# Kernel tuning notes

Hardware: AMD Instinct MI355X
Metric: run time of the kernel (lower is better)

Reference implementation:

```python
import jax, jax.numpy as jnp
import numpy as np

ITERATIONS = 4

def setup_inputs() -> dict:
    key = jax.random.key(0)
    x = jax.random.normal(key, (16, 8192, 256), dtype=jnp.float32)
    return {"x": x}

def reference(x):
    # x: [B, S, D]; whiten features (last dim) using stats over axis=1 (sequence)
    B, S, D = x.shape
    m = jnp.mean(x, axis=1, keepdims=True)          # [B, 1, D]
    xn = x - m                                      # centered
    # covariance: [B, D, D]
    sigma = jnp.einsum('bsd,bse->bde', xn, xn) / (S - 1)
    # Newton-Schulz iteration for inverse matrix square root
    tr = jnp.trace(sigma, axis1=1, axis2=2)[:, None, None]   # [B,1,1]
    sigma_n = sigma / tr
    eye = jnp.eye(D, dtype=x.dtype)
    P = jnp.broadcast_to(eye, (B, D, D))
    for _ in range(ITERATIONS):
        P = 1.5 * P - 0.5 * (P @ P @ P @ sigma_n)
    wm = P / jnp.sqrt(tr)                           # whitening matrix [B, D, D]
    decorrelated = jnp.einsum('bsd,bde->bse', xn, wm)
    return decorrelated
```

## Files before the change

### kernel.cpp

```cpp
#include <hip/hip_runtime.h>

#define BB 16
#define SS 8192
#define DD 256

typedef __attribute__((ext_vector_type(8))) short bf16x8;
typedef __attribute__((ext_vector_type(4))) short bf16x4;
typedef __attribute__((ext_vector_type(4))) float f32x4;

union frag_u { bf16x8 v8; bf16x4 v4[2]; };

__device__ __forceinline__ unsigned short f2bf(float f) {
    union { float f; unsigned u; } v; v.f = f;
    unsigned r = v.u + 0x7FFFu + ((v.u >> 16) & 1u);
    return (unsigned short)(r >> 16);
}
__device__ __forceinline__ float bf2f(unsigned short u) {
    union { unsigned u; float f; } cv; cv.u = (unsigned)u << 16; return cv.f;
}
__device__ __forceinline__ unsigned pack2(float a, float b) {
    return (unsigned)f2bf(a) | ((unsigned)f2bf(b) << 16);
}
__device__ __forceinline__ bf16x8 ldfrag(const unsigned short* p) {
    frag_u f;
    f.v4[0] = *(const bf16x4*)(p);
    f.v4[1] = *(const bf16x4*)(p + 4);
    return f.v8;
}
__device__ __forceinline__ void split_bf(float w, unsigned short& hi, unsigned short& lo) {
    hi = f2bf(w);
    lo = f2bf(w - bf2f(hi));
}

#define LTS 40

__global__ __launch_bounds__(512) void moment_kernel(const float* __restrict__ x,
                                                     float* __restrict__ partial,
                                                     float* __restrict__ sumx8) {
    const int kc = blockIdx.x;
    const int nh = blockIdx.y;
    const int b  = blockIdx.z;
    const float* xb = x + ((size_t)b * SS + (size_t)kc * 1024) * DD;

    __shared__ unsigned short Lt0[256 * LTS];
    __shared__ unsigned short Lt1[256 * LTS];
    __shared__ float csh[8 * 256];

    const int tid  = threadIdx.x;
    const int wave = tid >> 6;
    const int lane = tid & 63;
    const int lc   = lane & 15;
    const int lq   = lane >> 4;

    const int mrow0 = (wave & 3) * 64;
    const int ncol0 = nh * 128 + (wave >> 2) * 64;

    const int sg = tid >> 6;
    const int dg = tid & 63;
    const float* xt = xb + (size_t)(sg * 4) * DD + dg;

    f32x4 acc[4][4];
#pragma unroll
    for (int mi = 0; mi < 4; ++mi)
#pragma unroll
        for (int ni = 0; ni < 4; ++ni) acc[mi][ni] = (f32x4){0.f, 0.f, 0.f, 0.f};
    float cs[4] = {0.f, 0.f, 0.f, 0.f};

    float va[16], vb[16];

    auto LOAD = [&](float* v, int t) {
#pragma unroll
        for (int i = 0; i < 4; ++i)
#pragma unroll
            for (int j = 0; j < 4; ++j)
                v[i * 4 + j] = xt[(size_t)(t * 32 + i) * DD + 64 * j];
    };
    auto STAGE = [&](const float* v, unsigned short* Lw) {
        if (nh == 0) {
#pragma unroll
            for (int j = 0; j < 4; ++j)
                cs[j] += v[j] + v[4 + j] + v[8 + j] + v[12 + j];
        }
#pragma unroll
        for (int j = 0; j < 4; ++j) {
            uint2 w;
            w.x = pack2(v[j], v[4 + j]);
            w.y = pack2(v[8 + j], v[12 + j]);
            *(uint2*)&Lw[(dg + 64 * j) * LTS + sg * 4] = w;
        }
    };
    auto COMPUTE = [&](const unsigned short* Lr) {
        bf16x8 af[4], bfr[4];
#pragma unroll
        for (int mi = 0; mi < 4; ++mi)
            af[mi] = *(const bf16x8*)&Lr[(mrow0 + mi * 16 + lc) * LTS + lq * 8];
#pragma unroll
        for (int ni = 0; ni < 4; ++ni)
            bfr[ni] = *(const bf16x8*)&Lr[(ncol0 + ni * 16 + lc) * LTS + lq * 8];
#pragma unroll
        for (int mi = 0; mi < 4; ++mi)
#pragma unroll
            for (int ni = 0; ni < 4; ++ni)
                acc[mi][ni] = __builtin_amdgcn_mfma_f32_16x16x32_bf16(
                    af[mi], bfr[ni], acc[mi][ni], 0, 0, 0);
    };

    LOAD(va, 0);
    STAGE(va, Lt0);
    LOAD(vb, 1);
    __syncthreads();

    for (int tt = 0; tt < 16; ++tt) {
        const int t0 = 2 * tt;
        STAGE(vb, Lt1);
        if (t0 < 30) LOAD(va, t0 + 2);
        COMPUTE(Lt0);
        __syncthreads();
        if (t0 + 1 < 31) STAGE(va, Lt0);
        if (t0 + 1 < 30) LOAD(vb, t0 + 3);
        COMPUTE(Lt1);
        __syncthreads();
    }

    float* pp = partial + (size_t)(kc * 16 + b) * DD * DD;
#pragma unroll
    for (int mi = 0; mi < 4; ++mi)
#pragma unroll
        for (int ni = 0; ni < 4; ++ni) {
            const int row = mrow0 + mi * 16 + lq * 4;
            const int col = ncol0 + ni * 16 + lc;
#pragma unroll
            for (int r = 0; r < 4; ++r)
                pp[(size_t)(row + r) * DD + col] = acc[mi][ni][r];
        }

    if (nh == 0) {
        __syncthreads();
#pragma unroll
        for (int j = 0; j < 4; ++j) csh[sg * 256 + dg + 64 * j] = cs[j];
        __syncthreads();
        if (tid < 256) {
            float t0 = 0.f;
#pragma unroll
            for (int g = 0; g < 8; ++g) t0 += csh[g * 256 + tid];
            sumx8[(size_t)(kc * 16 + b) * DD + tid] = t0;
        }
    }
}

__global__ __launch_bounds__(256) void stats_kernel(const float* __restrict__ partial,
                                                    const float* __restrict__ sumx8,
                                                    float* __restrict__ m,
                                                    float* __restrict__ trbuf) {
    const int b = blockIdx.x;
    const int d = threadIdx.x;
    float sx = 0.f;
#pragma unroll
    for (int kc = 0; kc < 8; ++kc)
        sx += sumx8[(size_t)(kc * 16 + b) * DD + d];
    const float mean = sx * (1.0f / (float)SS);
    m[b * DD + d] = mean;
    float ds = 0.f;
#pragma unroll
    for (int kc = 0; kc < 8; ++kc)
        ds += partial[((size_t)(kc * 16 + b) * DD + d) * DD + d];
    const float diag = (ds - (float)SS * mean * mean) * (1.0f / (float)(SS - 1));
    __shared__ float red[256];
    red[d] = diag;
    __syncthreads();
    for (int off = 128; off > 0; off >>= 1) {
        if (d < off) red[d] += red[d + off];
        __syncthreads();
    }
    if (d == 0) {
        const float tr = red[0];
        trbuf[b]      = tr;
        trbuf[16 + b] = rsqrtf(tr);
        trbuf[32 + b] = 1.0f / tr;
    }
}

__global__ __launch_bounds__(256) void sigman_kernel(const float* __restrict__ partial,
                                                     const float* __restrict__ m,
                                                     const float* __restrict__ trbuf,
                                                     float* __restrict__ Xa) {
    const int b = blockIdx.y;
    const int d = blockIdx.x;
    const int e = threadIdx.x;
    const float itr = trbuf[32 + b];
    const float md = m[b * DD + d];
    const float me = m[b * DD + e];
    float s = 0.f;
#pragma unroll
    for (int kc = 0; kc < 8; ++kc)
        s += partial[((size_t)(kc * 16 + b) * DD + d) * DD + e];
    Xa[(size_t)b * DD * DD + (size_t)d * DD + e] =
        (s - (float)SS * md * me) * (1.0f / (float)(SS - 1)) * itr;
}

#define BTS 72
__global__ __launch_bounds__(256) void bmm_mfma(
    const float* __restrict__ A0, const float* __restrict__ B0, float* __restrict__ C0,
    int ta0, int tb0,
    const float* __restrict__ A1, const float* __restrict__ B1, float* __restrict__ C1,
    int ta1, int tb1) {
    const int by  = blockIdx.y;
    const int set = by >> 4;
    const int bb  = by & 15;
    const float* Ag = (set ? A1 : A0) + (size_t)bb * DD * DD;
    const float* Bg = (set ? B1 : B0) + (size_t)bb * DD * DD;
    float*       Cg = (set ? C1 : C0) + (size_t)bb * DD * DD;
    const int TA = set ? ta1 : ta0;
    const int TB = set ? tb1 : tb0;

    const int m0 = (blockIdx.x >> 2) * 64;
    const int n0 = (blockIdx.x & 3) * 64;

    __shared__ unsigned short Ahi[2][64 * BTS];
    __shared__ unsigned short Alo[2][64 * BTS];
    __shared__ unsigned short Bhi[2][64 * BTS];
    __shared__ unsigned short Blo[2][64 * BTS];

    const int tid  = threadIdx.x;
    const int wave = tid >> 6;
    const int lane = tid & 63;
    const int lc = lane & 15, lq = lane >> 4;
    const int mrow0 = (wave & 1) * 32;
    const int ncol0 = (wave >> 1) * 32;

    const int r  = tid >> 2;
    const int kl = (tid & 3) * 4;
    const float* Arow = Ag + (size_t)(m0 + r) * DD + kl;
    const float* Brow = Bg + (size_t)(n0 + r) * DD + kl;

    f32x4 acc[2][2];
#pragma unroll
    for (int mi = 0; mi < 2; ++mi)
#pragma unroll
        for (int ni = 0; ni < 2; ++ni) acc[mi][ni] = (f32x4){0.f, 0.f, 0.f, 0.f};

    float4 va0[4], vb0[4], va1[4], vb1[4];

    auto LOADC = [&](float4* va, float4* vb, int c) {
#pragma unroll
        for (int i = 0; i < 4; ++i) va[i] = *(const float4*)(Arow + c * 64 + i * 16);
#pragma unroll
        for (int i = 0; i < 4; ++i) vb[i] = *(const float4*)(Brow + c * 64 + i * 16);
    };
    auto STAGE_SIDE = [&](const float4* v, unsigned short* Shi, unsigned short* Slo,
                          int c, int gmn, int tflag) {
#pragma unroll
        for (int i = 0; i < 4; ++i) {
            float xv[4] = {v[i].x, v[i].y, v[i].z, v[i].w};
            unsigned short h[4], l[4];
#pragma unroll
            for (int j = 0; j < 4; ++j) {
                float wv = xv[j];
                if (tflag) {
                    const int gk = c * 64 + kl + i * 16 + j;
                    wv = ((gk == gmn) ? 1.5f : 0.0f) - 0.5f * wv;
                }
                split_bf(wv, h[j], l[j]);
            }
            unsigned short* ph = &Shi[r * BTS + kl + i * 16];
            *(unsigned*)&ph[0] = (unsigned)h[0] | ((unsigned)h[1] << 16);
            *(unsigned*)&ph[2] = (unsigned)h[2] | ((unsigned)h[3] << 16);
            unsigned short* pl = &Slo[r * BTS + kl + i * 16];
            *(unsigned*)&pl[0] = (unsigned)l[0] | ((unsigned)l[1] << 16);
            *(unsigned*)&pl[2] = (unsigned)l[2] | ((unsigned)l[3] << 16);
        }
    };
    auto STAGE = [&](const float4* va, const float4* vb, int c, int buf) {
        STAGE_SIDE(va, Ahi[buf], Alo[buf], c, m0 + r, TA);
        STAGE_SIDE(vb, Bhi[buf], Blo[buf], c, n0 + r, TB);
    };
    auto COMPUTE = [&](int buf) {
#pragma unroll
        for (int ks = 0; ks < 2; ++ks) {
            bf16x8 ah[2], al[2], bh[2], bl[2];
#pragma unroll
            for (int mi = 0; mi < 2; ++mi) {
                const int off = (mrow0 + mi * 16 + lc) * BTS + ks * 32 + lq * 8;
                ah[mi] = *(const bf16x8*)&Ahi[buf][off];
                al[mi] = *(const bf16x8*)&Alo[buf][off];
            }
#pragma unroll
            for (int ni = 0; ni < 2; ++ni) {
                const int off = (ncol0 + ni * 16 + lc) * BTS + ks * 32 + lq * 8;
                bh[ni] = *(const bf16x8*)&Bhi[buf][off];
                bl[ni] = *(const bf16x8*)&Blo[buf][off];
            }
#pragma unroll
            for (int mi = 0; mi < 2; ++mi)
#pragma unroll
                for (int ni = 0; ni < 2; ++ni) {
                    acc[mi][ni] = __builtin_amdgcn_mfma_f32_16x16x32_bf16(
                        al[mi], bh[ni], acc[mi][ni], 0, 0, 0);
                    acc[mi][ni] = __builtin_amdgcn_mfma_f32_16x16x32_bf16(
                        ah[mi], bl[ni], acc[mi][ni], 0, 0, 0);
                    acc[mi][ni] = __builtin_amdgcn_mfma_f32_16x16x32_bf16(
                        ah[mi], bh[ni], acc[mi][ni], 0, 0, 0);
                }
        }
    };

    LOADC(va0, vb0, 0);
    STAGE(va0, vb0, 0, 0);
    LOADC(va1, vb1, 1);
    __syncthreads();
#pragma unroll
    for (int cc = 0; cc < 2; ++cc) {
        const int c0 = 2 * cc;
        STAGE(va1, vb1, c0 + 1, 1);
        if (c0 + 2 < 4) LOADC(va0, vb0, c0 + 2);
        COMPUTE(0);
        __syncthreads();
        if (c0 + 2 < 4) STAGE(va0, vb0, c0 + 2, 0);
        if (c0 + 3 < 4) LOADC(va1, vb1, c0 + 3);
        COMPUTE(1);
        __syncthreads();
    }

#pragma unroll
    for (int mi = 0; mi < 2; ++mi)
#pragma unroll
        for (int ni = 0; ni < 2; ++ni) {
            const int row = m0 + mrow0 + mi * 16 + lq * 4;
            const int col = n0 + ncol0 + ni * 16 + lc;
#pragma unroll
            for (int rr = 0; rr < 4; ++rr)
                Cg[(size_t)(row + rr) * DD + col] = acc[mi][ni][rr];
        }
}

#define BSS 260
__global__ __launch_bounds__(512) void apply_kernel(const float* __restrict__ x,
                                                    const float* __restrict__ P,
                                                    const float* __restrict__ m,
                                                    const float* __restrict__ trbuf,
                                                    float* __restrict__ out) {
    const int st = blockIdx.x;
    const int nh = blockIdx.y;
    const int b  = blockIdx.z;
    const int s0 = st * 256;
    const int n0 = nh * 128;
    const float rs = trbuf[16 + b];
    const float* xb = x + (size_t)b * SS * DD;
    const float* Pb = P + (size_t)b * DD * DD;
    const float* mb = m + b * DD;
    float* ob = out + (size_t)b * SS * DD;

    __shared__ unsigned short Bs[128 * BSS];
    __shared__ unsigned short As0[256 * LTS];
    __shared__ unsigned short As1[256 * LTS];
    __shared__ float corr[128];

    const int tid  = threadIdx.x;
    const int wave = tid >> 6;
    const int lane = tid & 63;
    const int lc = lane & 15, lq = lane >> 4;
    const int mrow0 = (wave & 3) * 64;
    const int ncol0 = (wave >> 2) * 64;

    {
        const int r = tid >> 2, h = tid & 3;
        const float* prow = Pb + (size_t)(n0 + r) * DD + h * 64;
        unsigned short* brow = &Bs[r * BSS + h * 64];
#pragma unroll
        for (int i = 0; i < 16; ++i) {
            float4 pv = *(const float4*)(prow + i * 4);
            *(unsigned*)&brow[i * 4]     = pack2(pv.x * rs, pv.y * rs);
            *(unsigned*)&brow[i * 4 + 2] = pack2(pv.z * rs, pv.w * rs);
        }
    }
    __syncthreads();

    if (tid < 128) {
        float s = 0.f;
        for (int k = 0; k < 256; ++k)
            s += mb[k] * bf2f(Bs[tid * BSS + k]);
        corr[tid] = s;
    }

    f32x4 acc[4][4];
#pragma unroll
    for (int mi = 0; mi < 4; ++mi)
#pragma unroll
        for (int ni = 0; ni < 4; ++ni) acc[mi][ni] = (f32x4){0.f, 0.f, 0.f, 0.f};

    const int r8 = tid >> 3;
    const int d4 = (tid & 7) * 4;
    const float* xt = xb + (size_t)(s0 + r8) * DD + d4;

    float4 va[4], vb[4];

    auto LOAD = [&](float4* v, int t) {
#pragma unroll
        for (int i = 0; i < 4; ++i)
            v[i] = *(const float4*)(xt + (size_t)t * 32 + (size_t)i * 64 * DD);
    };
    auto STAGE = [&](const float4* v, unsigned short* Aw) {
#pragma unroll
        for (int i = 0; i < 4; ++i) {
            uint2 w;
            w.x = pack2(v[i].x, v[i].y);
            w.y = pack2(v[i].z, v[i].w);
            *(uint2*)&Aw[(r8 + i * 64) * LTS + d4] = w;
        }
    };
    auto COMPUTE = [&](const unsigned short* Ar, int t) {
        const int k0 = t * 32;
        bf16x8 af[4], bfr[4];
#pragma unroll
        for (int mi = 0; mi < 4; ++mi)
            af[mi] = *(const bf16x8*)&Ar[(mrow0 + mi * 16 + lc) * LTS + lq * 8];
#pragma unroll
        for (int ni = 0; ni < 4; ++ni)
            bfr[ni] = ldfrag(&Bs[(ncol0 + ni * 16 + lc) * BSS + k0 + lq * 8]);
#pragma unroll
        for (int mi = 0; mi < 4; ++mi)
#pragma unroll
            for (int ni = 0; ni < 4; ++ni)
                acc[mi][ni] = __builtin_amdgcn_mfma_f32_16x16x32_bf16(
                    af[mi], bfr[ni], acc[mi][ni], 0, 0, 0);
    };

    LOAD(va, 0);
    STAGE(va, As0);
    LOAD(vb, 1);
    __syncthreads();

#pragma unroll
    for (int tt = 0; tt < 4; ++tt) {
        const int t0 = 2 * tt;
        STAGE(vb, As1);
        if (t0 < 6) LOAD(va, t0 + 2);
        COMPUTE(As0, t0);
        __syncthreads();
        if (t0 + 2 < 8) STAGE(va, As0);
        if (t0 + 3 < 8) LOAD(vb, t0 + 3);
        COMPUTE(As1, t0 + 1);
        __syncthreads();
    }

#pragma unroll
    for (int mi = 0; mi < 4; ++mi)
#pragma unroll
        for (int ni = 0; ni < 4; ++ni) {
            const int row = s0 + mrow0 + mi * 16 + lq * 4;
            const int col = n0 + ncol0 + ni * 16 + lc;
            const float cv = corr[ncol0 + ni * 16 + lc];
#pragma unroll
            for (int r = 0; r < 4; ++r)
                ob[(size_t)(row + r) * DD + col] = acc[mi][ni][r] - cv;
        }
}

extern "C" void kernel_launch(void* const* d_in, const int* in_sizes, int n_in,
                              void* d_out, int out_size, void* d_ws, size_t ws_size,
                              hipStream_t stream) {
    const float* x = (const float*)d_in[0];
    float* out = (float*)d_out;
    float* ws = (float*)d_ws;

    const size_t MAT = (size_t)BB * DD * DD;
    float* partial = ws;
    float* sumx8 = partial + 8 * MAT;
    float* m     = sumx8 + 8 * BB * DD;
    float* trbuf = m + BB * DD;
    float* Xa    = trbuf + 64;
    float* Xb    = Xa + MAT;
    float* T     = Xb + MAT;
    float* Pa    = T + MAT;
    float* Pb    = Pa + MAT;

    moment_kernel<<<dim3(8, 2, 16), 512, 0, stream>>>(x, partial, sumx8);
    stats_kernel<<<16, 256, 0, stream>>>(partial, sumx8, m, trbuf);
    sigman_kernel<<<dim3(256, 16), 256, 0, stream>>>(partial, m, trbuf, Xa);

    bmm_mfma<<<dim3(16, 16), 256, 0, stream>>>(Xa, Xa, T, 1, 1,
                                               Xa, Xa, T, 1, 1);
    bmm_mfma<<<dim3(16, 16), 256, 0, stream>>>(Xa, T, Xb, 0, 0,
                                               Xa, T, Xb, 0, 0);
    bmm_mfma<<<dim3(16, 32), 256, 0, stream>>>(Xa, Xb, Pa, 1, 1,
                                               Xb, Xb, T, 1, 1);
    bmm_mfma<<<dim3(16, 16), 256, 0, stream>>>(Xb, T, Xa, 0, 0,
                                               Xb, T, Xa, 0, 0);
    bmm_mfma<<<dim3(16, 32), 256, 0, stream>>>(Pa, Xa, Pb, 0, 1,
                                               Xa, Xa, T, 1, 1);
    bmm_mfma<<<dim3(16, 16), 256, 0, stream>>>(Xa, T, Xb, 0, 0,
                                               Xa, T, Xb, 0, 0);
    bmm_mfma<<<dim3(16, 16), 256, 0, stream>>>(Pb, Xb, Pa, 0, 1,
                                               Pb, Xb, Pa, 0, 1);

    apply_kernel<<<dim3(32, 2, 16), 512, 0, stream>>>(x, Pa, m, trbuf, out);
}
```

Measured before the change: 372.8 us.

## Fuse Newton-Schulz matmul chain into one cooperative kernel and retile apply

Replaces the seven separate batched-matmul launches with a single cooperative kernel. It runs nine 64x64-tile passes separated by grid-wide syncs, using 512 threads per block and 8-element staging per thread. The goal is to remove per-launch overhead and tail gaps between the small matmuls. The trade-off is that independent matmul pairs now run one after another and each pass pays a grid-barrier cost. The apply kernel is also retiled to 128-row tiles with 256 threads and a single-buffered A tile, and its B stride is padded so fragments load as aligned 16-byte reads.

```diff
diff --git a/kernel.cpp b/kernel.cpp
--- a/kernel.cpp
+++ b/kernel.cpp
@@ -1,4 +1,7 @@
 #include <hip/hip_runtime.h>
+#include <hip/hip_cooperative_groups.h>
+
+namespace cg = cooperative_groups;
 
 #define BB 16
 #define SS 8192
@@ -7,8 +10,6 @@
 typedef __attribute__((ext_vector_type(8))) short bf16x8;
 typedef __attribute__((ext_vector_type(4))) short bf16x4;
 typedef __attribute__((ext_vector_type(4))) float f32x4;
-
-union frag_u { bf16x8 v8; bf16x4 v4[2]; };
 
 __device__ __forceinline__ unsigned short f2bf(float f) {
     union { float f; unsigned u; } v; v.f = f;
@@ -20,12 +21,6 @@
 }
 __device__ __forceinline__ unsigned pack2(float a, float b) {
     return (unsigned)f2bf(a) | ((unsigned)f2bf(b) << 16);
-}
-__device__ __forceinline__ bf16x8 ldfrag(const unsigned short* p) {
-    frag_u f;
-    f.v4[0] = *(const bf16x4*)(p);
-    f.v4[1] = *(const bf16x4*)(p + 4);
-    return f.v8;
 }
 __device__ __forceinline__ void split_bf(float w, unsigned short& hi, unsigned short& lo) {
     hi = f2bf(w);
@@ -199,142 +194,141 @@
 }
 
 #define BTS 72
-__global__ __launch_bounds__(256) void bmm_mfma(
-    const float* __restrict__ A0, const float* __restrict__ B0, float* __restrict__ C0,
-    int ta0, int tb0,
-    const float* __restrict__ A1, const float* __restrict__ B1, float* __restrict__ C1,
-    int ta1, int tb1) {
-    const int by  = blockIdx.y;
-    const int set = by >> 4;
-    const int bb  = by & 15;
-    const float* Ag = (set ? A1 : A0) + (size_t)bb * DD * DD;
-    const float* Bg = (set ? B1 : B0) + (size_t)bb * DD * DD;
-    float*       Cg = (set ? C1 : C0) + (size_t)bb * DD * DD;
-    const int TA = set ? ta1 : ta0;
-    const int TB = set ? tb1 : tb0;
-
-    const int m0 = (blockIdx.x >> 2) * 64;
-    const int n0 = (blockIdx.x & 3) * 64;
-
-    __shared__ unsigned short Ahi[2][64 * BTS];
-    __shared__ unsigned short Alo[2][64 * BTS];
-    __shared__ unsigned short Bhi[2][64 * BTS];
-    __shared__ unsigned short Blo[2][64 * BTS];
-
+__device__ __forceinline__ void bmm_pass(const float* Ag, const float* Bg, float* Cg,
+                                         int TA, int TB, int tile,
+                                         unsigned short* sm) {
     const int tid  = threadIdx.x;
     const int wave = tid >> 6;
     const int lane = tid & 63;
     const int lc = lane & 15, lq = lane >> 4;
+    const int m0 = (tile >> 2) * 64, n0 = (tile & 3) * 64;
     const int mrow0 = (wave & 1) * 32;
-    const int ncol0 = (wave >> 1) * 32;
-
-    const int r  = tid >> 2;
-    const int kl = (tid & 3) * 4;
-    const float* Arow = Ag + (size_t)(m0 + r) * DD + kl;
-    const float* Brow = Bg + (size_t)(n0 + r) * DD + kl;
-
-    f32x4 acc[2][2];
-#pragma unroll
-    for (int mi = 0; mi < 2; ++mi)
-#pragma unroll
-        for (int ni = 0; ni < 2; ++ni) acc[mi][ni] = (f32x4){0.f, 0.f, 0.f, 0.f};
-
-    float4 va0[4], vb0[4], va1[4], vb1[4];
-
-    auto LOADC = [&](float4* va, float4* vb, int c) {
-#pragma unroll
-        for (int i = 0; i < 4; ++i) va[i] = *(const float4*)(Arow + c * 64 + i * 16);
-#pragma unroll
-        for (int i = 0; i < 4; ++i) vb[i] = *(const float4*)(Brow + c * 64 + i * 16);
-    };
-    auto STAGE_SIDE = [&](const float4* v, unsigned short* Shi, unsigned short* Slo,
-                          int c, int gmn, int tflag) {
-#pragma unroll
-        for (int i = 0; i < 4; ++i) {
-            float xv[4] = {v[i].x, v[i].y, v[i].z, v[i].w};
-            unsigned short h[4], l[4];
-#pragma unroll
-            for (int j = 0; j < 4; ++j) {
-                float wv = xv[j];
-                if (tflag) {
-                    const int gk = c * 64 + kl + i * 16 + j;
-                    wv = ((gk == gmn) ? 1.5f : 0.0f) - 0.5f * wv;
-                }
-                split_bf(wv, h[j], l[j]);
+    const int ncol0 = (wave >> 1) * 16;
+
+    const int r  = tid >> 3;
+    const int k8 = (tid & 7) * 8;
+    const float* Arow = Ag + (size_t)(m0 + r) * DD + k8;
+    const float* Brow = Bg + (size_t)(n0 + r) * DD + k8;
+
+    unsigned short* SL[2][4];
+#pragma unroll
+    for (int bf = 0; bf < 2; ++bf)
+#pragma unroll
+        for (int w = 0; w < 4; ++w) SL[bf][w] = sm + (size_t)(bf * 4 + w) * 64 * BTS;
+
+    f32x4 acc[2];
+    acc[0] = (f32x4){0.f, 0.f, 0.f, 0.f};
+    acc[1] = (f32x4){0.f, 0.f, 0.f, 0.f};
+
+    float4 a0[2], b0[2], a1[2], b1[2];
+
+    auto LOADC = [&](float4* a, float4* b, int c) {
+        a[0] = *(const float4*)(Arow + c * 64);
+        a[1] = *(const float4*)(Arow + c * 64 + 4);
+        b[0] = *(const float4*)(Brow + c * 64);
+        b[1] = *(const float4*)(Brow + c * 64 + 4);
+    };
+    auto STAGE1 = [&](const float4* v, unsigned short* Shi, unsigned short* Slo,
+                      int c, int gmn, int tf) {
+        const float* vf = (const float*)v;
+        unsigned short h[8], l[8];
+#pragma unroll
+        for (int j = 0; j < 8; ++j) {
+            float wv = vf[j];
+            if (tf) {
+                const int gk = c * 64 + k8 + j;
+                wv = ((gk == gmn) ? 1.5f : 0.0f) - 0.5f * wv;
             }
-            unsigned short* ph = &Shi[r * BTS + kl + i * 16];
-            *(unsigned*)&ph[0] = (unsigned)h[0] | ((unsigned)h[1] << 16);
-            *(unsigned*)&ph[2] = (unsigned)h[2] | ((unsigned)h[3] << 16);
-            unsigned short* pl = &Slo[r * BTS + kl + i * 16];
-            *(unsigned*)&pl[0] = (unsigned)l[0] | ((unsigned)l[1] << 16);
-            *(unsigned*)&pl[2] = (unsigned)l[2] | ((unsigned)l[3] << 16);
-        }
-    };
-    auto STAGE = [&](const float4* va, const float4* vb, int c, int buf) {
-        STAGE_SIDE(va, Ahi[buf], Alo[buf], c, m0 + r, TA);
-        STAGE_SIDE(vb, Bhi[buf], Blo[buf], c, n0 + r, TB);
-    };
-    auto COMPUTE = [&](int buf) {
+            split_bf(wv, h[j], l[j]);
+        }
+        uint4 uh, ul;
+        uh.x = (unsigned)h[0] | ((unsigned)h[1] << 16);
+        uh.y = (unsigned)h[2] | ((unsigned)h[3] << 16);
+        uh.z = (unsigned)h[4] | ((unsigned)h[5] << 16);
+        uh.w = (unsigned)h[6] | ((unsigned)h[7] << 16);
+        ul.x = (unsigned)l[0] | ((unsigned)l[1] << 16);
+        ul.y = (unsigned)l[2] | ((unsigned)l[3] << 16);
+        ul.z = (unsigned)l[4] | ((unsigned)l[5] << 16);
+        ul.w = (unsigned)l[6] | ((unsigned)l[7] << 16);
+        *(uint4*)&Shi[r * BTS + k8] = uh;
+        *(uint4*)&Slo[r * BTS + k8] = ul;
+    };
+    auto STAGE = [&](const float4* a, const float4* b, int c, int bf) {
+        STAGE1(a, SL[bf][0], SL[bf][1], c, m0 + r, TA);
+        STAGE1(b, SL[bf][2], SL[bf][3], c, n0 + r, TB);
+    };
+    auto COMPUTE = [&](int bf) {
 #pragma unroll
         for (int ks = 0; ks < 2; ++ks) {
-            bf16x8 ah[2], al[2], bh[2], bl[2];
-#pragma unroll
-            for (int mi = 0; mi < 2; ++mi) {
-                const int off = (mrow0 + mi * 16 + lc) * BTS + ks * 32 + lq * 8;
-                ah[mi] = *(const bf16x8*)&Ahi[buf][off];
-                al[mi] = *(const bf16x8*)&Alo[buf][off];
-            }
-#pragma unroll
-            for (int ni = 0; ni < 2; ++ni) {
-                const int off = (ncol0 + ni * 16 + lc) * BTS + ks * 32 + lq * 8;
-                bh[ni] = *(const bf16x8*)&Bhi[buf][off];
-                bl[ni] = *(const bf16x8*)&Blo[buf][off];
-            }
-#pragma unroll
-            for (int mi = 0; mi < 2; ++mi)
-#pragma unroll
-                for (int ni = 0; ni < 2; ++ni) {
-                    acc[mi][ni] = __builtin_amdgcn_mfma_f32_16x16x32_bf16(
-                        al[mi], bh[ni], acc[mi][ni], 0, 0, 0);
-                    acc[mi][ni] = __builtin_amdgcn_mfma_f32_16x16x32_bf16(
-                        ah[mi], bl[ni], acc[mi][ni], 0, 0, 0);
-                    acc[mi][ni] = __builtin_amdgcn_mfma_f32_16x16x32_bf16(
-                        ah[mi], bh[ni], acc[mi][ni], 0, 0, 0);
-                }
-        }
-    };
-
-    LOADC(va0, vb0, 0);
-    STAGE(va0, vb0, 0, 0);
-    LOADC(va1, vb1, 1);
+            const int ko = ks * 32 + lq * 8;
+            bf16x8 ah0 = *(const bf16x8*)&SL[bf][0][(mrow0 + lc) * BTS + ko];
+            bf16x8 ah1 = *(const bf16x8*)&SL[bf][0][(mrow0 + 16 + lc) * BTS + ko];
+            bf16x8 al0 = *(const bf16x8*)&SL[bf][1][(mrow0 + lc) * BTS + ko];
+            bf16x8 al1 = *(const bf16x8*)&SL[bf][1][(mrow0 + 16 + lc) * BTS + ko];
+            bf16x8 bh  = *(const bf16x8*)&SL[bf][2][(ncol0 + lc) * BTS + ko];
+            bf16x8 bl  = *(const bf16x8*)&SL[bf][3][(ncol0 + lc) * BTS + ko];
+            acc[0] = __builtin_amdgcn_mfma_f32_16x16x32_bf16(al0, bh, acc[0], 0, 0, 0);
+            acc[0] = __builtin_amdgcn_mfma_f32_16x16x32_bf16(ah0, bl, acc[0], 0, 0, 0);
+            acc[0] = __builtin_amdgcn_mfma_f32_16x16x32_bf16(ah0, bh, acc[0], 0, 0, 0);
+            acc[1] = __builtin_amdgcn_mfma_f32_16x16x32_bf16(al1, bh, acc[1], 0, 0, 0);
+            acc[1] = __builtin_amdgcn_mfma_f32_16x16x32_bf16(ah1, bl, acc[1], 0, 0, 0);
+            acc[1] = __builtin_amdgcn_mfma_f32_16x16x32_bf16(ah1, bh, acc[1], 0, 0, 0);
+        }
+    };
+
+    LOADC(a0, b0, 0);
+    STAGE(a0, b0, 0, 0);
+    LOADC(a1, b1, 1);
     __syncthreads();
 #pragma unroll
     for (int cc = 0; cc < 2; ++cc) {
         const int c0 = 2 * cc;
-        STAGE(va1, vb1, c0 + 1, 1);
-        if (c0 + 2 < 4) LOADC(va0, vb0, c0 + 2);
+        STAGE(a1, b1, c0 + 1, 1);
+        if (c0 + 2 < 4) LOADC(a0, b0, c0 + 2);
         COMPUTE(0);
         __syncthreads();
-        if (c0 + 2 < 4) STAGE(va0, vb0, c0 + 2, 0);
-        if (c0 + 3 < 4) LOADC(va1, vb1, c0 + 3);
+        if (c0 + 2 < 4) STAGE(a0, b0, c0 + 2, 0);
+        if (c0 + 3 < 4) LOADC(a1, b1, c0 + 3);
         COMPUTE(1);
         __syncthreads();
     }
 
 #pragma unroll
-    for (int mi = 0; mi < 2; ++mi)
-#pragma unroll
-        for (int ni = 0; ni < 2; ++ni) {
-            const int row = m0 + mrow0 + mi * 16 + lq * 4;
-            const int col = n0 + ncol0 + ni * 16 + lc;
-#pragma unroll
-            for (int rr = 0; rr < 4; ++rr)
-                Cg[(size_t)(row + rr) * DD + col] = acc[mi][ni][rr];
-        }
-}
-
-#define BSS 260
-__global__ __launch_bounds__(512) void apply_kernel(const float* __restrict__ x,
+    for (int mi = 0; mi < 2; ++mi) {
+        const int row = m0 + mrow0 + mi * 16 + lq * 4;
+        const int col = n0 + ncol0 + lc;
+#pragma unroll
+        for (int rr = 0; rr < 4; ++rr)
+            Cg[(size_t)(row + rr) * DD + col] = acc[mi][rr];
+    }
+}
+
+__global__ __launch_bounds__(512) void ns_chain(float* Xa, float* Xb, float* T,
+                                                float* Pa, float* Pb) {
+    cg::grid_group grid = cg::this_grid();
+    __shared__ __align__(16) unsigned short sm[8 * 64 * BTS];
+
+    const int bx   = blockIdx.x;
+    const int tile = bx & 15;
+    const size_t off = (size_t)(bx >> 4) * DD * DD;
+
+    const float* Al[9] = {Xa, Xa, Xa, Xb, Xb, Pa, Xa, Xa, Pb};
+    const float* Bl[9] = {Xa, T,  Xb, Xb, T,  Xa, Xa, T,  Xb};
+    float*       Cl[9] = {T,  Xb, Pa, T,  Xa, Pb, T,  Xb, Pa};
+    const int   TAl[9] = {1, 0, 1, 1, 0, 0, 1, 0, 0};
+    const int   TBl[9] = {1, 0, 1, 1, 0, 1, 1, 0, 1};
+
+    for (int p = 0; p < 9; ++p) {
+        if (p) {
+            __threadfence();
+            grid.sync();
+        }
+        bmm_pass(Al[p] + off, Bl[p] + off, Cl[p] + off, TAl[p], TBl[p], tile, sm);
+    }
+}
+
+#define BSS 264
+__global__ __launch_bounds__(256) void apply_kernel(const float* __restrict__ x,
                                                     const float* __restrict__ P,
                                                     const float* __restrict__ m,
                                                     const float* __restrict__ trbuf,
@@ -342,7 +336,7 @@
     const int st = blockIdx.x;
     const int nh = blockIdx.y;
     const int b  = blockIdx.z;
-    const int s0 = st * 256;
+    const int s0 = st * 128;
     const int n0 = nh * 128;
     const float rs = trbuf[16 + b];
     const float* xb = x + (size_t)b * SS * DD;
@@ -351,23 +345,22 @@
     float* ob = out + (size_t)b * SS * DD;
 
     __shared__ unsigned short Bs[128 * BSS];
-    __shared__ unsigned short As0[256 * LTS];
-    __shared__ unsigned short As1[256 * LTS];
+    __shared__ unsigned short As[128 * LTS];
     __shared__ float corr[128];
 
     const int tid  = threadIdx.x;
     const int wave = tid >> 6;
     const int lane = tid & 63;
     const int lc = lane & 15, lq = lane >> 4;
-    const int mrow0 = (wave & 3) * 64;
-    const int ncol0 = (wave >> 2) * 64;
+    const int mrow0 = (wave & 1) * 64;
+    const int ncol0 = (wave >> 1) * 64;
 
     {
-        const int r = tid >> 2, h = tid & 3;
-        const float* prow = Pb + (size_t)(n0 + r) * DD + h * 64;
-        unsigned short* brow = &Bs[r * BSS + h * 64];
-#pragma unroll
-        for (int i = 0; i < 16; ++i) {
+        const int r = tid >> 1, h = tid & 1;
+        const float* prow = Pb + (size_t)(n0 + r) * DD + h * 128;
+        unsigned short* brow = &Bs[r * BSS + h * 128];
+#pragma unroll
+        for (int i = 0; i < 32; ++i) {
             float4 pv = *(const float4*)(prow + i * 4);
             *(unsigned*)&brow[i * 4]     = pack2(pv.x * rs, pv.y * rs);
             *(unsigned*)&brow[i * 4 + 2] = pack2(pv.z * rs, pv.w * rs);
@@ -397,26 +390,26 @@
     auto LOAD = [&](float4* v, int t) {
 #pragma unroll
         for (int i = 0; i < 4; ++i)
-            v[i] = *(const float4*)(xt + (size_t)t * 32 + (size_t)i * 64 * DD);
-    };
-    auto STAGE = [&](const float4* v, unsigned short* Aw) {
+            v[i] = *(const float4*)(xt + (size_t)t * 32 + (size_t)i * 32 * DD);
+    };
+    auto STAGE = [&](const float4* v) {
 #pragma unroll
         for (int i = 0; i < 4; ++i) {
             uint2 w;
             w.x = pack2(v[i].x, v[i].y);
             w.y = pack2(v[i].z, v[i].w);
-            *(uint2*)&Aw[(r8 + i * 64) * LTS + d4] = w;
-        }
-    };
-    auto COMPUTE = [&](const unsigned short* Ar, int t) {
+            *(uint2*)&As[(r8 + i * 32) * LTS + d4] = w;
+        }
+    };
+    auto COMPUTE = [&](int t) {
         const int k0 = t * 32;
         bf16x8 af[4], bfr[4];
 #pragma unroll
         for (int mi = 0; mi < 4; ++mi)
-            af[mi] = *(const bf16x8*)&Ar[(mrow0 + mi * 16 + lc) * LTS + lq * 8];
+            af[mi] = *(const bf16x8*)&As[(mrow0 + mi * 16 + lc) * LTS + lq * 8];
 #pragma unroll
         for (int ni = 0; ni < 4; ++ni)
-            bfr[ni] = ldfrag(&Bs[(ncol0 + ni * 16 + lc) * BSS + k0 + lq * 8]);
+            bfr[ni] = *(const bf16x8*)&Bs[(ncol0 + ni * 16 + lc) * BSS + k0 + lq * 8];
 #pragma unroll
         for (int mi = 0; mi < 4; ++mi)
 #pragma unroll
@@ -426,21 +419,19 @@
     };
 
     LOAD(va, 0);
-    STAGE(va, As0);
-    LOAD(vb, 1);
-    __syncthreads();
-
 #pragma unroll
     for (int tt = 0; tt < 4; ++tt) {
         const int t0 = 2 * tt;
-        STAGE(vb, As1);
-        if (t0 < 6) LOAD(va, t0 + 2);
-        COMPUTE(As0, t0);
-        __syncthreads();
-        if (t0 + 2 < 8) STAGE(va, As0);
-        if (t0 + 3 < 8) LOAD(vb, t0 + 3);
-        COMPUTE(As1, t0 + 1);
-        __syncthreads();
+        __syncthreads();
+        STAGE(va);
+        if (t0 + 1 < 8) LOAD(vb, t0 + 1);
+        __syncthreads();
+        COMPUTE(t0);
+        __syncthreads();
+        STAGE(vb);
+        if (t0 + 2 < 8) LOAD(va, t0 + 2);
+        __syncthreads();
+        COMPUTE(t0 + 1);
     }
 
 #pragma unroll
@@ -478,20 +469,10 @@
     stats_kernel<<<16, 256, 0, stream>>>(partial, sumx8, m, trbuf);
     sigman_kernel<<<dim3(256, 16), 256, 0, stream>>>(partial, m, trbuf, Xa);
 
-    bmm_mfma<<<dim3(16, 16), 256, 0, stream>>>(Xa, Xa, T, 1, 1,
-                                               Xa, Xa, T, 1, 1);
-    bmm_mfma<<<dim3(16, 16), 256, 0, stream>>>(Xa, T, Xb, 0, 0,
-                                               Xa, T, Xb, 0, 0);
-    bmm_mfma<<<dim3(16, 32), 256, 0, stream>>>(Xa, Xb, Pa, 1, 1,
-                                               Xb, Xb, T, 1, 1);
-    bmm_mfma<<<dim3(16, 16), 256, 0, stream>>>(Xb, T, Xa, 0, 0,
-                                               Xb, T, Xa, 0, 0);
-    bmm_mfma<<<dim3(16, 32), 256, 0, stream>>>(Pa, Xa, Pb, 0, 1,
-                                               Xa, Xa, T, 1, 1);
-    bmm_mfma<<<dim3(16, 16), 256, 0, stream>>>(Xa, T, Xb, 0, 0,
-                                               Xa, T, Xb, 0, 0);
-    bmm_mfma<<<dim3(16, 16), 256, 0, stream>>>(Pb, Xb, Pa, 0, 1,
-                                               Pb, Xb, Pa, 0, 1);
-
-    apply_kernel<<<dim3(32, 2, 16), 512, 0, stream>>>(x, Pa, m, trbuf, out);
-}
+    {
+        void* args[] = {&Xa, &Xb, &T, &Pa, &Pb};
+        hipLaunchCooperativeKernel(ns_chain, dim3(256), dim3(512), args, 0, stream);
+    }
+
+    apply_kernel<<<dim3(64, 2, 16), 256, 0, stream>>>(x, Pa, m, trbuf, out);
+}
```

Result: slower. 987.3 us (+164.8%).

## Shrink apply kernel tiles to 128 rows with single LDS buffer

Applied to the files above, without the earlier changes.

The apply kernel now processes 128 sequence rows per block with 256 threads (4 waves) instead of 256 rows with 512 threads, doubling the grid and dropping the double-buffered A tile for a single buffer with extra barriers. The B tile stride is padded to 264 so B fragments can be read with a single 16-byte LDS load instead of two 8-byte loads. The intent is lower LDS use per block, more resident blocks and better tail balance. The cost is that each block re-converts the P slice for half as many rows and loses compute/staging overlap within the block. The bmm kernel also issues its second global load before the first staging.

```diff
diff --git a/kernel.cpp b/kernel.cpp
--- a/kernel.cpp
+++ b/kernel.cpp
@@ -7,8 +7,6 @@
 typedef __attribute__((ext_vector_type(8))) short bf16x8;
 typedef __attribute__((ext_vector_type(4))) short bf16x4;
 typedef __attribute__((ext_vector_type(4))) float f32x4;
-
-union frag_u { bf16x8 v8; bf16x4 v4[2]; };
 
 __device__ __forceinline__ unsigned short f2bf(float f) {
     union { float f; unsigned u; } v; v.f = f;
@@ -20,12 +18,6 @@
 }
 __device__ __forceinline__ unsigned pack2(float a, float b) {
     return (unsigned)f2bf(a) | ((unsigned)f2bf(b) << 16);
-}
-__device__ __forceinline__ bf16x8 ldfrag(const unsigned short* p) {
-    frag_u f;
-    f.v4[0] = *(const bf16x4*)(p);
-    f.v4[1] = *(const bf16x4*)(p + 4);
-    return f.v8;
 }
 __device__ __forceinline__ void split_bf(float w, unsigned short& hi, unsigned short& lo) {
     hi = f2bf(w);
@@ -305,8 +297,8 @@
     };
 
     LOADC(va0, vb0, 0);
+    LOADC(va1, vb1, 1);
     STAGE(va0, vb0, 0, 0);
-    LOADC(va1, vb1, 1);
     __syncthreads();
 #pragma unroll
     for (int cc = 0; cc < 2; ++cc) {
@@ -333,8 +325,8 @@
         }
 }
 
-#define BSS 260
-__global__ __launch_bounds__(512) void apply_kernel(const float* __restrict__ x,
+#define BSS 264
+__global__ __launch_bounds__(256) void apply_kernel(const float* __restrict__ x,
                                                     const float* __restrict__ P,
                                                     const float* __restrict__ m,
                                                     const float* __restrict__ trbuf,
@@ -342,7 +334,7 @@
     const int st = blockIdx.x;
     const int nh = blockIdx.y;
     const int b  = blockIdx.z;
-    const int s0 = st * 256;
+    const int s0 = st * 128;
     const int n0 = nh * 128;
     const float rs = trbuf[16 + b];
     const float* xb = x + (size_t)b * SS * DD;
@@ -351,23 +343,22 @@
     float* ob = out + (size_t)b * SS * DD;
 
     __shared__ unsigned short Bs[128 * BSS];
-    __shared__ unsigned short As0[256 * LTS];
-    __shared__ unsigned short As1[256 * LTS];
+    __shared__ unsigned short As[128 * LTS];
     __shared__ float corr[128];
 
     const int tid  = threadIdx.x;
     const int wave = tid >> 6;
     const int lane = tid & 63;
     const int lc = lane & 15, lq = lane >> 4;
-    const int mrow0 = (wave & 3) * 64;
-    const int ncol0 = (wave >> 2) * 64;
+    const int mrow0 = (wave & 1) * 64;
+    const int ncol0 = (wave >> 1) * 64;
 
     {
-        const int r = tid >> 2, h = tid & 3;
-        const float* prow = Pb + (size_t)(n0 + r) * DD + h * 64;
-        unsigned short* brow = &Bs[r * BSS + h * 64];
-#pragma unroll
-        for (int i = 0; i < 16; ++i) {
+        const int r = tid >> 1, h = tid & 1;
+        const float* prow = Pb + (size_t)(n0 + r) * DD + h * 128;
+        unsigned short* brow = &Bs[r * BSS + h * 128];
+#pragma unroll
+        for (int i = 0; i < 32; ++i) {
             float4 pv = *(const float4*)(prow + i * 4);
             *(unsigned*)&brow[i * 4]     = pack2(pv.x * rs, pv.y * rs);
             *(unsigned*)&brow[i * 4 + 2] = pack2(pv.z * rs, pv.w * rs);
@@ -397,26 +388,26 @@
     auto LOAD = [&](float4* v, int t) {
 #pragma unroll
         for (int i = 0; i < 4; ++i)
-            v[i] = *(const float4*)(xt + (size_t)t * 32 + (size_t)i * 64 * DD);
-    };
-    auto STAGE = [&](const float4* v, unsigned short* Aw) {
+            v[i] = *(const float4*)(xt + (size_t)t * 32 + (size_t)i * 32 * DD);
+    };
+    auto STAGE = [&](const float4* v) {
 #pragma unroll
         for (int i = 0; i < 4; ++i) {
             uint2 w;
             w.x = pack2(v[i].x, v[i].y);
             w.y = pack2(v[i].z, v[i].w);
-            *(uint2*)&Aw[(r8 + i * 64) * LTS + d4] = w;
-        }
-    };
-    auto COMPUTE = [&](const unsigned short* Ar, int t) {
+            *(uint2*)&As[(r8 + i * 32) * LTS + d4] = w;
+        }
+    };
+    auto COMPUTE = [&](int t) {
         const int k0 = t * 32;
         bf16x8 af[4], bfr[4];
 #pragma unroll
         for (int mi = 0; mi < 4; ++mi)
-            af[mi] = *(const bf16x8*)&Ar[(mrow0 + mi * 16 + lc) * LTS + lq * 8];
+            af[mi] = *(const bf16x8*)&As[(mrow0 + mi * 16 + lc) * LTS + lq * 8];
 #pragma unroll
         for (int ni = 0; ni < 4; ++ni)
-            bfr[ni] = ldfrag(&Bs[(ncol0 + ni * 16 + lc) * BSS + k0 + lq * 8]);
+            bfr[ni] = *(const bf16x8*)&Bs[(ncol0 + ni * 16 + lc) * BSS + k0 + lq * 8];
 #pragma unroll
         for (int mi = 0; mi < 4; ++mi)
 #pragma unroll
@@ -426,21 +417,19 @@
     };
 
     LOAD(va, 0);
-    STAGE(va, As0);
-    LOAD(vb, 1);
-    __syncthreads();
-
 #pragma unroll
     for (int tt = 0; tt < 4; ++tt) {
         const int t0 = 2 * tt;
-        STAGE(vb, As1);
-        if (t0 < 6) LOAD(va, t0 + 2);
-        COMPUTE(As0, t0);
-        __syncthreads();
-        if (t0 + 2 < 8) STAGE(va, As0);
-        if (t0 + 3 < 8) LOAD(vb, t0 + 3);
-        COMPUTE(As1, t0 + 1);
-        __syncthreads();
+        __syncthreads();
+        STAGE(va);
+        if (t0 + 1 < 8) LOAD(vb, t0 + 1);
+        __syncthreads();
+        COMPUTE(t0);
+        __syncthreads();
+        STAGE(vb);
+        if (t0 + 2 < 8) LOAD(va, t0 + 2);
+        __syncthreads();
+        COMPUTE(t0 + 1);
     }
 
 #pragma unroll
@@ -493,5 +482,5 @@
     bmm_mfma<<<dim3(16, 16), 256, 0, stream>>>(Pb, Xb, Pa, 0, 1,
                                                Pb, Xb, Pa, 0, 1);
 
-    apply_kernel<<<dim3(32, 2, 16), 512, 0, stream>>>(x, Pa, m, trbuf, out);
-}
+    apply_kernel<<<dim3(64, 2, 16), 256, 0, stream>>>(x, Pa, m, trbuf, out);
+}
```

Measured after the change: 379.1 us. About the same (+1.7%).
